# Kernel optimization log

Measured on AMD Instinct MI355X. Metric: run time of the kernel, lower is better.

Reference implementation:

```python
import jax, jax.numpy as jnp
import numpy as np

NB, NA, NC, NH, NW = 128, 5, 80, 28, 28
NT = 50
ANCHORS = jnp.array([2.8, 4.8, 5.1, 10.2, 6.4, 16.3, 9.2, 19.8, 14.1, 23.7], dtype=jnp.float32)
ANCHOR_W = ANCHORS[0::2]  # [NA]
ANCHOR_H = ANCHORS[1::2]
OBJECT_SCALE = 5.0
NOOBJECT_SCALE = 1.0
CLASS_SCALE = 1.0
COORD_SCALE = 1.0
SIL_THRESH = 0.6


def iou_cxcywh(b1, b2):
    # center-format IoU, matches bbox_ious(x1y1x2y2=False); inputs broadcastable (...,4)
    x1, y1, w1, h1 = b1[..., 0], b1[..., 1], b1[..., 2], b1[..., 3]
    x2, y2, w2, h2 = b2[..., 0], b2[..., 1], b2[..., 2], b2[..., 3]
    mx = jnp.minimum(x1 - w1 / 2, x2 - w2 / 2)
    Mx = jnp.maximum(x1 + w1 / 2, x2 + w2 / 2)
    my = jnp.minimum(y1 - h1 / 2, y2 - h2 / 2)
    My = jnp.maximum(y1 + h1 / 2, y2 + h2 / 2)
    cw = w1 + w2 - (Mx - mx)
    ch = h1 + h2 - (My - my)
    inter = jnp.where((cw > 0) & (ch > 0), cw * ch, 0.0)
    union = w1 * h1 + w2 * h2 - inter
    return inter / union


def build_targets(pred_boxes, target):
    # pred_boxes: [NB, NA, NH, NW, 4] grid-unit cxcywh (already detached)
    tgt = target.reshape(NB, NT, 5)
    gcls = tgt[..., 0]
    gx = tgt[..., 1] * NW
    gy = tgt[..., 2] * NH
    gw = tgt[..., 3] * NW
    gh = tgt[..., 4] * NH
    gt_boxes = jnp.stack([gx, gy, gw, gh], -1)  # [NB, NT, 4]

    # silence mask: any-GT IoU > thresh -> conf_mask 0, else noobject_scale
    pb = pred_boxes.reshape(NB, NA * NH * NW, 4)
    ious = iou_cxcywh(pb[:, :, None, :], gt_boxes[:, None, :, :])  # [NB, nAnchors, NT]
    max_iou = jnp.max(ious, axis=2)
    conf_mask0 = jnp.where(max_iou > SIL_THRESH, 0.0, NOOBJECT_SCALE).reshape(NB, NA, NH, NW)

    # best anchor per GT by wh-only IoU at origin
    z_na = jnp.zeros((NA,), jnp.float32)
    anc = jnp.stack([z_na, z_na, ANCHOR_W, ANCHOR_H], -1)  # [NA,4]
    zg = jnp.zeros_like(gw)
    gt_wh = jnp.stack([zg, zg, gw, gh], -1)  # [NB,NT,4]
    a_iou = iou_cxcywh(gt_wh[:, :, None, :], anc[None, None, :, :])  # [NB,NT,NA]
    best_n = jnp.argmax(a_iou, axis=2)  # [NB,NT] (first max, matches strict > loop)

    gi = jnp.floor(gx).astype(jnp.int32)
    gj = jnp.floor(gy).astype(jnp.int32)
    flat_idx = ((jnp.arange(NB)[:, None] * NA + best_n) * NH + gj) * NW + gi  # [NB,NT]

    assigned_pred = pred_boxes.reshape(NB * NA * NH * NW, 4)[flat_idx]  # [NB,NT,4]
    iou_gt_pred = iou_cxcywh(gt_boxes, assigned_pred)  # [NB,NT]
    aw = ANCHOR_W[best_n]
    ah = ANCHOR_H[best_n]

    idx = flat_idx.reshape(-1)
    grid0 = jnp.zeros((NB * NA * NH * NW,), jnp.float32)

    def sc(init_flat, v):
        return init_flat.at[idx].set(v.reshape(-1)).reshape(NB, NA, NH, NW)

    ones = jnp.ones((NB, NT), jnp.float32)
    coord_mask = sc(grid0, ones)
    cls_mask = sc(grid0, ones)
    conf_mask = sc(conf_mask0.reshape(-1), jnp.full((NB, NT), OBJECT_SCALE, jnp.float32))
    tx = sc(grid0, gx - gi.astype(jnp.float32))
    ty = sc(grid0, gy - gj.astype(jnp.float32))
    tw = sc(grid0, jnp.log(gw / aw))
    th = sc(grid0, jnp.log(gh / ah))
    tconf = sc(grid0, iou_gt_pred)
    tcls = sc(grid0, gcls)
    return coord_mask, conf_mask, cls_mask, tx, ty, tw, th, tconf, tcls


def _smooth_l1_sum(a, b):
    d = a - b
    ad = jnp.abs(d)
    return jnp.sum(jnp.where(ad < 1.0, 0.5 * d * d, ad - 0.5))


def _forward(output, target):
    out = output.reshape(NB, NA, 5 + NC, NH, NW)
    x = jax.nn.sigmoid(out[:, :, 0])
    y = jax.nn.sigmoid(out[:, :, 1])
    w = out[:, :, 2]
    h = out[:, :, 3]
    conf = jax.nn.sigmoid(out[:, :, 4])
    cls_logits = jnp.transpose(out[:, :, 5:], (0, 1, 3, 4, 2))  # [NB,NA,NH,NW,NC]

    gx = jnp.arange(NW, dtype=jnp.float32)[None, None, None, :]
    gy = jnp.arange(NH, dtype=jnp.float32)[None, None, :, None]
    sg = jax.lax.stop_gradient
    px = sg(x) + gx
    py = sg(y) + gy
    pw = jnp.exp(sg(w)) * ANCHOR_W[None, :, None, None]
    ph = jnp.exp(sg(h)) * ANCHOR_H[None, :, None, None]
    pred_boxes = jnp.stack([px, py, pw, ph], -1)  # [NB,NA,NH,NW,4]

    bt = jax.lax.stop_gradient(build_targets(pred_boxes, target))
    coord_mask, conf_mask, cls_mask, tx, ty, tw, th, tconf, tcls = bt
    conf_mask = jnp.sqrt(conf_mask)

    loss_x = COORD_SCALE * _smooth_l1_sum(x * coord_mask, tx * coord_mask) / 2.0
    loss_y = COORD_SCALE * _smooth_l1_sum(y * coord_mask, ty * coord_mask) / 2.0
    loss_w = COORD_SCALE * _smooth_l1_sum(w * coord_mask, tw * coord_mask) / 2.0
    loss_h = COORD_SCALE * _smooth_l1_sum(h * coord_mask, th * coord_mask) / 2.0
    loss_conf = jnp.sum((conf * conf_mask - tconf * conf_mask) ** 2) / 2.0

    # focal loss (gamma=2, alpha=1, sum reduction) over cells with cls_mask==1
    logp = jax.nn.log_softmax(cls_logits, axis=-1)
    logp_t = jnp.take_along_axis(logp, tcls[..., None].astype(jnp.int32), axis=-1)[..., 0]
    p_t = jnp.exp(logp_t)
    focal = -((1.0 - p_t) ** 2) * logp_t
    loss_cls = CLASS_SCALE * jnp.sum(cls_mask * focal)

    return loss_x + loss_y + loss_w + loss_h + loss_conf + loss_cls


def setup_inputs() -> dict:
    key = jax.random.key(0)
    k1, k2, k3 = jax.random.split(key, 3)
    output = jax.random.normal(k1, (NB, NA * (5 + NC), NH, NW), dtype=jnp.float32)
    u = jax.random.uniform(k2, (NB, NT, 4), dtype=jnp.float32)
    xy = 0.1 + 0.8 * u[..., :2]   # x in (0.1,0.9) -> never 0, no early break
    wh = 0.05 + 0.45 * u[..., 2:]
    cls_id = jax.random.randint(k3, (NB, NT, 1), 0, NC).astype(jnp.float32)
    target = jnp.concatenate([cls_id, xy, wh], axis=-1).reshape(NB, NT * 5)
    return {"output": output, "target": target}


def reference(output, target):
    return _forward(output, target)
```

## Files before the change

### kernel.cpp

```cpp
#include <hip/hip_runtime.h>
#include <math.h>

#define NBB 128
#define NAA 5
#define NCC 80
#define NHH 28
#define NWW 28
#define NTT 50
#define CH  85
#define HW  784
#define CELLS 3920

__constant__ float c_AW[5] = {2.8f, 5.1f, 6.4f, 9.2f, 14.1f};
__constant__ float c_AH[5] = {4.8f, 10.2f, 16.3f, 19.8f, 23.7f};

__device__ __forceinline__ float sigmoidf_(float x) {
    return 1.0f / (1.0f + __expf(-x));
}

__device__ __forceinline__ float smooth_l1(float d) {
    float ad = fabsf(d);
    return (ad < 1.0f) ? 0.5f * d * d : ad - 0.5f;
}

__global__ __launch_bounds__(1024) void region_loss_fused(
    const float* __restrict__ out, const float* __restrict__ tgt,
    float* __restrict__ d_out)
{
    __shared__ float4 boxS[NTT];
    __shared__ float  s6[NTT];
    __shared__ float2 ctS[NTT];
    __shared__ int    rCell[NTT];
    __shared__ float  rTx[NTT], rTy[NTT], rTw[NTT], rTh[NTT];
    __shared__ int    rCls[NTT];
    __shared__ unsigned char rActive[NTT];
    __shared__ float  wred[16];

    const int b   = blockIdx.y;
    const int tid = threadIdx.x;

    if (tid < NTT) {
        const float* tp = tgt + b * NTT * 5 + tid * 5;
        float cls = tp[0];
        float gx = tp[1] * NWW;
        float gy = tp[2] * NHH;
        float gw = tp[3] * NWW;
        float gh = tp[4] * NHH;
        float ga = gw * gh;

        boxS[tid] = make_float4(gx - gw * 0.5f, gx + gw * 0.5f,
                                gy - gh * 0.5f, gy + gh * 0.5f);
        s6[tid] = 0.375f * ga;

        int best = 0; float bestI = -1.0f;
        #pragma unroll
        for (int a = 0; a < 5; ++a) {
            float inter = fminf(gw, c_AW[a]) * fminf(gh, c_AH[a]);
            float uni   = ga + c_AW[a] * c_AH[a] - inter;
            float iou   = inter / uni;
            if (iou > bestI) { bestI = iou; best = a; }
        }
        int gi = (int)floorf(gx);
        int gj = (int)floorf(gy);
        int cell = (best * NHH + gj) * NWW + gi;

        const float* op = out + ((size_t)(b * NAA + best) * CH) * HW + gj * NWW + gi;
        float px = sigmoidf_(op[0])      + (float)gi;
        float py = sigmoidf_(op[HW])     + (float)gj;
        float pw = __expf(op[2 * HW]) * c_AW[best];
        float ph = __expf(op[3 * HW]) * c_AH[best];

        float mx = fminf(px - pw * 0.5f, gx - gw * 0.5f);
        float Mx = fmaxf(px + pw * 0.5f, gx + gw * 0.5f);
        float my = fminf(py - ph * 0.5f, gy - gh * 0.5f);
        float My = fmaxf(py + ph * 0.5f, gy + gh * 0.5f);
        float cw  = pw + gw - (Mx - mx);
        float chh = ph + gh - (My - my);
        float inter = (cw > 0.f && chh > 0.f) ? cw * chh : 0.f;
        float uni   = pw * ph + ga - inter;

        rCell[tid] = cell;
        ctS[tid]   = make_float2(__int_as_float(cell), inter / uni);
        rTx[tid]   = gx - (float)gi;
        rTy[tid]   = gy - (float)gj;
        rTw[tid]   = __logf(gw / c_AW[best]);
        rTh[tid]   = __logf(gh / c_AH[best]);
        rCls[tid]  = (int)cls;
    }
    __syncthreads();

    if (tid < NTT) {
        int cell = rCell[tid];
        unsigned char active = 1;
        for (int t2 = tid + 1; t2 < NTT; ++t2)
            if (rCell[t2] == cell) active = 0;
        rActive[tid] = active;
    }

    const int cell = blockIdx.x * 1024 + tid;
    float term = 0.0f;

    if (cell < CELLS) {
        int a  = cell / HW;
        int hw = cell - a * HW;
        int wi = hw % NWW;
        int hj = hw / NWW;
        const float* op = out + ((size_t)(b * NAA + a) * CH) * HW + hw;

        float px   = sigmoidf_(op[0])  + (float)wi;
        float py   = sigmoidf_(op[HW]) + (float)hj;
        float pw   = __expf(op[2 * HW]) * c_AW[a];
        float ph   = __expf(op[3 * HW]) * c_AH[a];
        float conf = sigmoidf_(op[4 * HW]);

        float l1 = px - pw * 0.5f, r1 = px + pw * 0.5f;
        float t1 = py - ph * 0.5f, b1 = py + ph * 0.5f;
        float c1 = 0.375f * (pw * ph);

        bool flag = false, assigned = false;
        float tc = 0.f;
        #pragma unroll 5
        for (int j = 0; j < NTT; ++j) {
            float4 bx = boxS[j];
            float cw  = fminf(r1, bx.y) - fmaxf(l1, bx.x);
            float ch2 = fminf(b1, bx.w) - fmaxf(t1, bx.z);
            float inter = fmaxf(cw, 0.f) * fmaxf(ch2, 0.f);
            flag = flag || (inter > c1 + s6[j]);
            float2 c2 = ctS[j];
            bool hit = (__float_as_int(c2.x) == cell);
            assigned = assigned || hit;
            tc = hit ? c2.y : tc;
        }

        if (assigned) { float d = conf - tc; term = 2.5f * d * d; }
        else if (!flag) { term = 0.5f * conf * conf; }
    }

    const int wave = tid >> 6;
    const int lane = tid & 63;
    const int j    = blockIdx.x * 16 + wave;
    float contrib = 0.0f;

    __syncthreads();

    if (j < NTT && rActive[j]) {
        int rc = rCell[j];
        int a  = rc / HW;
        int hw = rc - a * HW;
        const float* op = out + ((size_t)(b * NAA + a) * CH) * HW + hw;

        float l0  = op[(5 + lane) * HW];
        float l1c = (lane < 16) ? op[(5 + 64 + lane) * HW] : -INFINITY;

        float m = fmaxf(l0, l1c);
        for (int o = 32; o >= 1; o >>= 1) m = fmaxf(m, __shfl_xor(m, o));
        float s = __expf(l0 - m) + ((lane < 16) ? __expf(l1c - m) : 0.0f);
        for (int o = 32; o >= 1; o >>= 1) s += __shfl_xor(s, o);

        int t = rCls[j];
        float lt = (t < 64) ? __shfl(l0, t) : __shfl(l1c, t - 64);
        float logpt = lt - m - __logf(s);
        float pt = __expf(logpt);
        float focal = -(1.0f - pt) * (1.0f - pt) * logpt;

        if (lane == 0) {
            float x = sigmoidf_(op[0]);
            float y = sigmoidf_(op[HW]);
            float w = op[2 * HW];
            float h = op[3 * HW];
            contrib = focal +
                      0.5f * (smooth_l1(x - rTx[j]) + smooth_l1(y - rTy[j]) +
                              smooth_l1(w - rTw[j]) + smooth_l1(h - rTh[j]));
        }
    }

    float v = term + ((lane == 0) ? contrib : 0.0f);
    #pragma unroll
    for (int o = 32; o >= 1; o >>= 1) v += __shfl_xor(v, o);
    if (lane == 0) wred[wave] = v;
    __syncthreads();
    if (tid == 0) {
        float s = 0.0f;
        #pragma unroll
        for (int w2 = 0; w2 < 16; ++w2) s += wred[w2];
        atomicAdd(d_out, s);
    }
}

extern "C" void kernel_launch(void* const* d_in, const int* in_sizes, int n_in,
                              void* d_out, int out_size, void* d_ws, size_t ws_size,
                              hipStream_t stream) {
    const float* out_p = (const float*)d_in[0];
    const float* tgt_p = (const float*)d_in[1];
    float* loss = (float*)d_out;

    hipMemsetAsync(loss, 0, (size_t)out_size * sizeof(float), stream);

    region_loss_fused<<<dim3(4, NBB), dim3(1024), 0, stream>>>(
        out_p, tgt_p, loss);
}
```

Baseline: 222.1 us.

## Process four cells per thread with shared assigned-cell table and 256-thread blocks

Shrinks blocks from 1024 to 256 threads, so each thread now handles four cells and reuses every GT box load from shared memory across them. The per-cell scan of GT assignments is replaced by a shared table of size CELLS, written only by the winning (last) GT for each cell and then looked up directly. Each wave handles up to four GTs for the class/coordinate loss. This cuts shared-memory loads per IoU test and removes the assignment compare from the inner loop, at the cost of about 16KB of shared memory per block, an extra barrier, and fewer threads to hide latency.

```diff
diff --git a/kernel.cpp b/kernel.cpp
--- a/kernel.cpp
+++ b/kernel.cpp
@@ -23,22 +23,27 @@
     return (ad < 1.0f) ? 0.5f * d * d : ad - 0.5f;
 }
 
-__global__ __launch_bounds__(1024) void region_loss_fused(
+__global__ __launch_bounds__(256) void region_loss_fused(
     const float* __restrict__ out, const float* __restrict__ tgt,
     float* __restrict__ d_out)
 {
+    __shared__ float  tcA[CELLS];
     __shared__ float4 boxS[NTT];
     __shared__ float  s6[NTT];
-    __shared__ float2 ctS[NTT];
     __shared__ int    rCell[NTT];
     __shared__ float  rTx[NTT], rTy[NTT], rTw[NTT], rTh[NTT];
     __shared__ int    rCls[NTT];
     __shared__ unsigned char rActive[NTT];
-    __shared__ float  wred[16];
+    __shared__ float  wred[4];
 
     const int b   = blockIdx.y;
+    const int bx  = blockIdx.x;
     const int tid = threadIdx.x;
 
+    for (int i = tid; i < CELLS; i += 256) tcA[i] = -1.0f;
+
+    float myTc = 0.0f;
+    int   myCell = -1;
     if (tid < NTT) {
         const float* tp = tgt + b * NTT * 5 + tid * 5;
         float cls = tp[0];
@@ -79,8 +84,9 @@
         float inter = (cw > 0.f && chh > 0.f) ? cw * chh : 0.f;
         float uni   = pw * ph + ga - inter;
 
+        myCell = cell;
+        myTc   = inter / uni;
         rCell[tid] = cell;
-        ctS[tid]   = make_float2(__int_as_float(cell), inter / uni);
         rTx[tid]   = gx - (float)gi;
         rTy[tid]   = gy - (float)gj;
         rTw[tid]   = __logf(gw / c_AW[best]);
@@ -90,101 +96,117 @@
     __syncthreads();
 
     if (tid < NTT) {
-        int cell = rCell[tid];
         unsigned char active = 1;
         for (int t2 = tid + 1; t2 < NTT; ++t2)
-            if (rCell[t2] == cell) active = 0;
+            if (rCell[t2] == myCell) active = 0;
         rActive[tid] = active;
-    }
-
-    const int cell = blockIdx.x * 1024 + tid;
-    float term = 0.0f;
-
-    if (cell < CELLS) {
-        int a  = cell / HW;
-        int hw = cell - a * HW;
-        int wi = hw % NWW;
-        int hj = hw / NWW;
-        const float* op = out + ((size_t)(b * NAA + a) * CH) * HW + hw;
-
-        float px   = sigmoidf_(op[0])  + (float)wi;
-        float py   = sigmoidf_(op[HW]) + (float)hj;
-        float pw   = __expf(op[2 * HW]) * c_AW[a];
-        float ph   = __expf(op[3 * HW]) * c_AH[a];
-        float conf = sigmoidf_(op[4 * HW]);
-
-        float l1 = px - pw * 0.5f, r1 = px + pw * 0.5f;
-        float t1 = py - ph * 0.5f, b1 = py + ph * 0.5f;
-        float c1 = 0.375f * (pw * ph);
-
-        bool flag = false, assigned = false;
-        float tc = 0.f;
-        #pragma unroll 5
-        for (int j = 0; j < NTT; ++j) {
-            float4 bx = boxS[j];
-            float cw  = fminf(r1, bx.y) - fmaxf(l1, bx.x);
-            float ch2 = fminf(b1, bx.w) - fmaxf(t1, bx.z);
-            float inter = fmaxf(cw, 0.f) * fmaxf(ch2, 0.f);
-            flag = flag || (inter > c1 + s6[j]);
-            float2 c2 = ctS[j];
-            bool hit = (__float_as_int(c2.x) == cell);
-            assigned = assigned || hit;
-            tc = hit ? c2.y : tc;
-        }
-
-        if (assigned) { float d = conf - tc; term = 2.5f * d * d; }
-        else if (!flag) { term = 0.5f * conf * conf; }
-    }
+        if (active) tcA[myCell] = myTc;
+    }
+    __syncthreads();
 
     const int wave = tid >> 6;
     const int lane = tid & 63;
-    const int j    = blockIdx.x * 16 + wave;
     float contrib = 0.0f;
 
-    __syncthreads();
-
-    if (j < NTT && rActive[j]) {
-        int rc = rCell[j];
-        int a  = rc / HW;
-        int hw = rc - a * HW;
-        const float* op = out + ((size_t)(b * NAA + a) * CH) * HW + hw;
-
-        float l0  = op[(5 + lane) * HW];
-        float l1c = (lane < 16) ? op[(5 + 64 + lane) * HW] : -INFINITY;
-
-        float m = fmaxf(l0, l1c);
-        for (int o = 32; o >= 1; o >>= 1) m = fmaxf(m, __shfl_xor(m, o));
-        float s = __expf(l0 - m) + ((lane < 16) ? __expf(l1c - m) : 0.0f);
-        for (int o = 32; o >= 1; o >>= 1) s += __shfl_xor(s, o);
-
-        int t = rCls[j];
-        float lt = (t < 64) ? __shfl(l0, t) : __shfl(l1c, t - 64);
-        float logpt = lt - m - __logf(s);
-        float pt = __expf(logpt);
-        float focal = -(1.0f - pt) * (1.0f - pt) * logpt;
-
-        if (lane == 0) {
-            float x = sigmoidf_(op[0]);
-            float y = sigmoidf_(op[HW]);
-            float w = op[2 * HW];
-            float h = op[3 * HW];
-            contrib = focal +
-                      0.5f * (smooth_l1(x - rTx[j]) + smooth_l1(y - rTy[j]) +
-                              smooth_l1(w - rTw[j]) + smooth_l1(h - rTh[j]));
-        }
-    }
-
-    float v = term + ((lane == 0) ? contrib : 0.0f);
+    #pragma unroll
+    for (int k = 0; k < 4; ++k) {
+        const int j = (bx * 4 + wave) + 16 * k;
+        if (j < NTT && rActive[j]) {
+            int rc = rCell[j];
+            int a  = rc / HW;
+            int hw = rc - a * HW;
+            const float* op = out + ((size_t)(b * NAA + a) * CH) * HW + hw;
+
+            float l0  = op[(5 + lane) * HW];
+            float l1c = (lane < 16) ? op[(5 + 64 + lane) * HW] : -INFINITY;
+
+            float m = fmaxf(l0, l1c);
+            for (int o = 32; o >= 1; o >>= 1) m = fmaxf(m, __shfl_xor(m, o));
+            float s = __expf(l0 - m) + ((lane < 16) ? __expf(l1c - m) : 0.0f);
+            for (int o = 32; o >= 1; o >>= 1) s += __shfl_xor(s, o);
+
+            int t = rCls[j];
+            float lt = (t < 64) ? __shfl(l0, t) : __shfl(l1c, t - 64);
+            float logpt = lt - m - __logf(s);
+            float pt = __expf(logpt);
+            float focal = -(1.0f - pt) * (1.0f - pt) * logpt;
+
+            if (lane == 0) {
+                float x = sigmoidf_(op[0]);
+                float y = sigmoidf_(op[HW]);
+                float w = op[2 * HW];
+                float h = op[3 * HW];
+                contrib += focal +
+                           0.5f * (smooth_l1(x - rTx[j]) + smooth_l1(y - rTy[j]) +
+                                   smooth_l1(w - rTw[j]) + smooth_l1(h - rTh[j]));
+            }
+        }
+    }
+
+    float l1c_[4], r1c_[4], t1c_[4], b1c_[4], c1c_[4], confc_[4];
+    bool  fl_[4];
+
+    #pragma unroll
+    for (int k = 0; k < 4; ++k) {
+        const int cell = bx * 1024 + (k << 8) + tid;
+        fl_[k] = false;
+        if (cell < CELLS) {
+            int a  = cell / HW;
+            int hw = cell - a * HW;
+            int wi = hw % NWW;
+            int hj = hw / NWW;
+            const float* op = out + ((size_t)(b * NAA + a) * CH) * HW + hw;
+
+            float px   = sigmoidf_(op[0])  + (float)wi;
+            float py   = sigmoidf_(op[HW]) + (float)hj;
+            float pw   = __expf(op[2 * HW]) * c_AW[a];
+            float ph   = __expf(op[3 * HW]) * c_AH[a];
+            confc_[k]  = sigmoidf_(op[4 * HW]);
+
+            l1c_[k] = px - pw * 0.5f;  r1c_[k] = px + pw * 0.5f;
+            t1c_[k] = py - ph * 0.5f;  b1c_[k] = py + ph * 0.5f;
+            c1c_[k] = 0.375f * (pw * ph);
+        } else {
+            l1c_[k] = 1e30f;  r1c_[k] = -1e30f;
+            t1c_[k] = 1e30f;  b1c_[k] = -1e30f;
+            c1c_[k] = 1e30f;  confc_[k] = 0.0f;
+        }
+    }
+
+    #pragma unroll 5
+    for (int j = 0; j < NTT; ++j) {
+        float4 bxj = boxS[j];
+        float  sj  = s6[j];
+        #pragma unroll
+        for (int k = 0; k < 4; ++k) {
+            float cw  = fminf(r1c_[k], bxj.y) - fmaxf(l1c_[k], bxj.x);
+            float ch2 = fminf(b1c_[k], bxj.w) - fmaxf(t1c_[k], bxj.z);
+            float inter = fmaxf(cw, 0.f) * fmaxf(ch2, 0.f);
+            fl_[k] = fl_[k] || (inter > c1c_[k] + sj);
+        }
+    }
+
+    float term = 0.0f;
+    #pragma unroll
+    for (int k = 0; k < 4; ++k) {
+        const int cell = bx * 1024 + (k << 8) + tid;
+        if (cell < CELLS) {
+            float tc = tcA[cell];
+            if (tc > -0.5f) {
+                float d = confc_[k] - tc; term += 2.5f * d * d;
+            } else if (!fl_[k]) {
+                term += 0.5f * confc_[k] * confc_[k];
+            }
+        }
+    }
+
+    float v = term + contrib;
     #pragma unroll
     for (int o = 32; o >= 1; o >>= 1) v += __shfl_xor(v, o);
     if (lane == 0) wred[wave] = v;
     __syncthreads();
-    if (tid == 0) {
-        float s = 0.0f;
-        #pragma unroll
-        for (int w2 = 0; w2 < 16; ++w2) s += wred[w2];
-        atomicAdd(d_out, s);
-    }
+    if (tid == 0)
+        atomicAdd(d_out, wred[0] + wred[1] + wred[2] + wred[3]);
 }
 
 extern "C" void kernel_launch(void* const* d_in, const int* in_sizes, int n_in,
@@ -196,6 +218,6 @@
 
     hipMemsetAsync(loss, 0, (size_t)out_size * sizeof(float), stream);
 
-    region_loss_fused<<<dim3(4, NBB), dim3(1024), 0, stream>>>(
+    region_loss_fused<<<dim3(4, NBB), dim3(256), 0, stream>>>(
         out_p, tgt_p, loss);
 }
```

After: 228.8 us. 1.03x slower.

## Replace per-cell GT scan with shared tc lookup table and readlane broadcasts

Applied to the files above, without the earlier changes.

Builds a per-batch shared-memory table indexed by cell, holding the target confidence of the assigned GT, so each cell does one lookup instead of comparing against all 50 GT cell ids in its loop. The silence-mask loop now keeps the GT box bounds in registers, one GT per lane, and broadcasts them with readlane instead of reading shared memory on every iteration, with a fully unrolled loop. Invalid cells get sentinel box values so every lane runs the loop without branching. The cost is a 3920-float table init per block, an extra barrier, and more shared memory, which may lower occupancy.

```diff
diff --git a/kernel.cpp b/kernel.cpp
--- a/kernel.cpp
+++ b/kernel.cpp
@@ -23,22 +23,30 @@
     return (ad < 1.0f) ? 0.5f * d * d : ad - 0.5f;
 }
 
+__device__ __forceinline__ float rdlane(float v, int l) {
+    return __uint_as_float(__builtin_amdgcn_readlane(__float_as_uint(v), l));
+}
+
 __global__ __launch_bounds__(1024) void region_loss_fused(
     const float* __restrict__ out, const float* __restrict__ tgt,
     float* __restrict__ d_out)
 {
-    __shared__ float4 boxS[NTT];
-    __shared__ float  s6[NTT];
-    __shared__ float2 ctS[NTT];
-    __shared__ int    rCell[NTT];
-    __shared__ float  rTx[NTT], rTy[NTT], rTw[NTT], rTh[NTT];
-    __shared__ int    rCls[NTT];
+    __shared__ float tcA[CELLS];
+    __shared__ float Lb[NTT], Rb[NTT], Tb[NTT], Bb[NTT], Sb[NTT];
+    __shared__ int   rCell[NTT];
+    __shared__ float rTx[NTT], rTy[NTT], rTw[NTT], rTh[NTT];
+    __shared__ int   rCls[NTT];
     __shared__ unsigned char rActive[NTT];
-    __shared__ float  wred[16];
+    __shared__ float wred[16];
 
     const int b   = blockIdx.y;
+    const int bx  = blockIdx.x;
     const int tid = threadIdx.x;
 
+    for (int i = tid; i < CELLS; i += 1024) tcA[i] = -1.0f;
+
+    float myTc = 0.0f;
+    int   myCell = -1;
     if (tid < NTT) {
         const float* tp = tgt + b * NTT * 5 + tid * 5;
         float cls = tp[0];
@@ -48,9 +56,11 @@
         float gh = tp[4] * NHH;
         float ga = gw * gh;
 
-        boxS[tid] = make_float4(gx - gw * 0.5f, gx + gw * 0.5f,
-                                gy - gh * 0.5f, gy + gh * 0.5f);
-        s6[tid] = 0.375f * ga;
+        Lb[tid] = gx - gw * 0.5f;
+        Rb[tid] = gx + gw * 0.5f;
+        Tb[tid] = gy - gh * 0.5f;
+        Bb[tid] = gy + gh * 0.5f;
+        Sb[tid] = 0.375f * ga;
 
         int best = 0; float bestI = -1.0f;
         #pragma unroll
@@ -79,8 +89,9 @@
         float inter = (cw > 0.f && chh > 0.f) ? cw * chh : 0.f;
         float uni   = pw * ph + ga - inter;
 
+        myCell = cell;
+        myTc   = inter / uni;
         rCell[tid] = cell;
-        ctS[tid]   = make_float2(__int_as_float(cell), inter / uni);
         rTx[tid]   = gx - (float)gi;
         rTy[tid]   = gy - (float)gj;
         rTw[tid]   = __logf(gw / c_AW[best]);
@@ -90,61 +101,74 @@
     __syncthreads();
 
     if (tid < NTT) {
-        int cell = rCell[tid];
         unsigned char active = 1;
         for (int t2 = tid + 1; t2 < NTT; ++t2)
-            if (rCell[t2] == cell) active = 0;
+            if (rCell[t2] == myCell) active = 0;
         rActive[tid] = active;
-    }
-
-    const int cell = blockIdx.x * 1024 + tid;
+        if (active) tcA[myCell] = myTc;
+    }
+    __syncthreads();
+
+    const int wave = tid >> 6;
+    const int lane = tid & 63;
+    const int ll   = (lane < NTT) ? lane : 0;
+    const float tL = Lb[ll], tR = Rb[ll], tT = Tb[ll], tB = Bb[ll], tS = Sb[ll];
+
+    const int cell = bx * 1024 + tid;
+    const bool valid = (cell < CELLS);
     float term = 0.0f;
 
-    if (cell < CELLS) {
+    float l1, r1, t1, b1, c1, conf;
+    if (valid) {
         int a  = cell / HW;
         int hw = cell - a * HW;
         int wi = hw % NWW;
         int hj = hw / NWW;
         const float* op = out + ((size_t)(b * NAA + a) * CH) * HW + hw;
 
-        float px   = sigmoidf_(op[0])  + (float)wi;
-        float py   = sigmoidf_(op[HW]) + (float)hj;
-        float pw   = __expf(op[2 * HW]) * c_AW[a];
-        float ph   = __expf(op[3 * HW]) * c_AH[a];
-        float conf = sigmoidf_(op[4 * HW]);
-
-        float l1 = px - pw * 0.5f, r1 = px + pw * 0.5f;
-        float t1 = py - ph * 0.5f, b1 = py + ph * 0.5f;
-        float c1 = 0.375f * (pw * ph);
-
-        bool flag = false, assigned = false;
-        float tc = 0.f;
-        #pragma unroll 5
-        for (int j = 0; j < NTT; ++j) {
-            float4 bx = boxS[j];
-            float cw  = fminf(r1, bx.y) - fmaxf(l1, bx.x);
-            float ch2 = fminf(b1, bx.w) - fmaxf(t1, bx.z);
-            float inter = fmaxf(cw, 0.f) * fmaxf(ch2, 0.f);
-            flag = flag || (inter > c1 + s6[j]);
-            float2 c2 = ctS[j];
-            bool hit = (__float_as_int(c2.x) == cell);
-            assigned = assigned || hit;
-            tc = hit ? c2.y : tc;
+        float px = sigmoidf_(op[0])  + (float)wi;
+        float py = sigmoidf_(op[HW]) + (float)hj;
+        float pw = __expf(op[2 * HW]) * c_AW[a];
+        float ph = __expf(op[3 * HW]) * c_AH[a];
+        conf     = sigmoidf_(op[4 * HW]);
+
+        l1 = px - pw * 0.5f;  r1 = px + pw * 0.5f;
+        t1 = py - ph * 0.5f;  b1 = py + ph * 0.5f;
+        c1 = 0.375f * (pw * ph);
+    } else {
+        l1 = 1e30f;  r1 = -1e30f;
+        t1 = 1e30f;  b1 = -1e30f;
+        c1 = 1e30f;  conf = 0.0f;
+    }
+
+    bool flag = false;
+    #pragma unroll
+    for (int j = 0; j < NTT; ++j) {
+        float Lj = rdlane(tL, j);
+        float Rj = rdlane(tR, j);
+        float Tj = rdlane(tT, j);
+        float Bj = rdlane(tB, j);
+        float Sj = rdlane(tS, j);
+        float cw  = fminf(r1, Rj) - fmaxf(l1, Lj);
+        float ch2 = fminf(b1, Bj) - fmaxf(t1, Tj);
+        float inter = fmaxf(cw, 0.f) * fmaxf(ch2, 0.f);
+        flag = flag || (inter > c1 + Sj);
+    }
+
+    if (valid) {
+        float tc = tcA[cell];
+        if (tc > -0.5f) {
+            float d = conf - tc; term = 2.5f * d * d;
+        } else if (!flag) {
+            term = 0.5f * conf * conf;
         }
-
-        if (assigned) { float d = conf - tc; term = 2.5f * d * d; }
-        else if (!flag) { term = 0.5f * conf * conf; }
-    }
-
-    const int wave = tid >> 6;
-    const int lane = tid & 63;
-    const int j    = blockIdx.x * 16 + wave;
+    }
+
+    const int j3 = bx * 16 + wave;
     float contrib = 0.0f;
 
-    __syncthreads();
-
-    if (j < NTT && rActive[j]) {
-        int rc = rCell[j];
+    if (j3 < NTT && rActive[j3]) {
+        int rc = rCell[j3];
         int a  = rc / HW;
         int hw = rc - a * HW;
         const float* op = out + ((size_t)(b * NAA + a) * CH) * HW + hw;
@@ -157,7 +181,7 @@
         float s = __expf(l0 - m) + ((lane < 16) ? __expf(l1c - m) : 0.0f);
         for (int o = 32; o >= 1; o >>= 1) s += __shfl_xor(s, o);
 
-        int t = rCls[j];
+        int t = rCls[j3];
         float lt = (t < 64) ? __shfl(l0, t) : __shfl(l1c, t - 64);
         float logpt = lt - m - __logf(s);
         float pt = __expf(logpt);
@@ -169,12 +193,12 @@
             float w = op[2 * HW];
             float h = op[3 * HW];
             contrib = focal +
-                      0.5f * (smooth_l1(x - rTx[j]) + smooth_l1(y - rTy[j]) +
-                              smooth_l1(w - rTw[j]) + smooth_l1(h - rTh[j]));
+                      0.5f * (smooth_l1(x - rTx[j3]) + smooth_l1(y - rTy[j3]) +
+                              smooth_l1(w - rTw[j3]) + smooth_l1(h - rTh[j3]));
         }
     }
 
-    float v = term + ((lane == 0) ? contrib : 0.0f);
+    float v = term + contrib;
     #pragma unroll
     for (int o = 32; o >= 1; o >>= 1) v += __shfl_xor(v, o);
     if (lane == 0) wred[wave] = v;
```

After: 227.2 us. +2.3%, slower.
